# Optimization experiments

Measured on AMD Instinct MI355X. Metric: run time of the kernel, lower is better.

## Reference

```python
import jax, jax.numpy as jnp
import numpy as np

HEADS = 16
DIM_HEAD = 64
SCALE = DIM_HEAD ** -0.5


def setup_inputs() -> dict:
    key = jax.random.key(0)
    ks = jax.random.split(key, 5)
    b, n, dim = 2, 2048, 1024
    inner = HEADS * DIM_HEAD  # 1024
    std = dim ** -0.5
    return {
        "x": jax.random.normal(ks[0], (b, n, dim), jnp.float32),
        "ln_gamma": jnp.ones((dim,), jnp.float32),
        "ln_beta": jnp.zeros((dim,), jnp.float32),
        "W_qk": jax.random.normal(ks[1], (dim, 2 * inner), jnp.float32) * std,
        "W_v": jax.random.normal(ks[2], (dim, inner), jnp.float32) * std,
        "W_out": jax.random.normal(ks[3], (inner, dim), jnp.float32) * std,
        "b_out": jnp.zeros((dim,), jnp.float32),
    }


def _layernorm(x, gamma, beta, eps=1e-5):
    mu = jnp.mean(x, axis=-1, keepdims=True)
    var = jnp.var(x, axis=-1, keepdims=True)
    return (x - mu) * jax.lax.rsqrt(var + eps) * gamma + beta


def reference(x, ln_gamma, ln_beta, W_qk, W_v, W_out, b_out):
    b, n, dim = x.shape
    h, d = HEADS, DIM_HEAD
    xn = _layernorm(x, ln_gamma, ln_beta)
    qk = xn @ W_qk                      # [b, n, 2*h*d]
    q, k = jnp.split(qk, 2, axis=-1)    # each [b, n, h*d]
    v = xn @ W_v                        # [b, n, h*d]
    # b n (h d) -> b h n d
    q = q.reshape(b, n, h, d).transpose(0, 2, 1, 3)
    k = k.reshape(b, n, h, d).transpose(0, 2, 1, 3)
    v = v.reshape(b, n, h, d).transpose(0, 2, 1, 3)
    dots = jnp.einsum('bhid,bhjd->bhij', q, k) * SCALE
    attn = jax.nn.softmax(dots, axis=-1)
    out = jnp.einsum('bhij,bhjd->bhid', attn, v)
    out = out.transpose(0, 2, 1, 3).reshape(b, n, h * d)
    return out @ W_out + b_out
```

## Files before the change

### kernel.cpp

```cpp
#include <hip/hip_runtime.h>

#define HEADS 16
#define DHEAD 64
#define BATCH 2
#define SEQ   2048
#define DIM   1024
#define ROWS  (BATCH*SEQ)
#define SCALE_LOG2E 0.180336880f

typedef short v8s __attribute__((ext_vector_type(8)));
typedef float v4f __attribute__((ext_vector_type(4)));

__device__ __forceinline__ float fast_exp2(float x) {
    return __builtin_amdgcn_exp2f(x);
}

__device__ __forceinline__ unsigned short f2bf(float f) {
    unsigned u = __float_as_uint(f);
    u += 0x7FFFu + ((u >> 16) & 1u);
    return (unsigned short)(u >> 16);
}

__device__ __forceinline__ unsigned pk_bf2(float hi, float lo) {
    return __builtin_amdgcn_perm(__float_as_uint(hi), __float_as_uint(lo), 0x07060302u);
}

#define GLDS16(g, l) __builtin_amdgcn_global_load_lds( \
    (__attribute__((address_space(1))) void*)(g), \
    (__attribute__((address_space(3))) void*)(l), 16, 0, 0)

__global__ __launch_bounds__(256) void ln_kernel(const float* __restrict__ x,
                                                 const float* __restrict__ gamma,
                                                 const float* __restrict__ beta,
                                                 unsigned short* __restrict__ xn) {
    int row = blockIdx.x;
    const float* xr = x + (size_t)row * DIM;
    int t = threadIdx.x;
    float4 v = *(const float4*)(xr + t * 4);
    float s  = v.x + v.y + v.z + v.w;
    float sq = v.x * v.x + v.y * v.y + v.z * v.z + v.w * v.w;
#pragma unroll
    for (int off = 32; off > 0; off >>= 1) {
        s  += __shfl_down(s,  off, 64);
        sq += __shfl_down(sq, off, 64);
    }
    __shared__ float ss[4], ssq[4];
    int wave = t >> 6, lane = t & 63;
    if (lane == 0) { ss[wave] = s; ssq[wave] = sq; }
    __syncthreads();
    float tot  = ss[0] + ss[1] + ss[2] + ss[3];
    float totq = ssq[0] + ssq[1] + ssq[2] + ssq[3];
    float mean = tot * (1.f / DIM);
    float var  = totq * (1.f / DIM) - mean * mean;
    float rstd = rsqrtf(var + 1e-5f);
    float4 g = *(const float4*)(gamma + t * 4);
    float4 bb = *(const float4*)(beta + t * 4);
    ushort4 o;
    o.x = f2bf((v.x - mean) * rstd * g.x + bb.x);
    o.y = f2bf((v.y - mean) * rstd * g.y + bb.y);
    o.z = f2bf((v.z - mean) * rstd * g.z + bb.z);
    o.w = f2bf((v.w - mean) * rstd * g.w + bb.w);
    *(ushort4*)(xn + (size_t)row * DIM + t * 4) = o;
}

__global__ __launch_bounds__(256) void tr_kernel(const float* __restrict__ W,
                                                 unsigned short* __restrict__ Wt,
                                                 int Kw, int Nw) {
    __shared__ float tile[64][65];
    int n0 = blockIdx.x * 64, k0 = blockIdx.y * 64;
    int tid = threadIdx.x;
#pragma unroll
    for (int l = 0; l < 4; ++l) {
        int kk = (tid >> 4) + l * 16;
        int nn = (tid & 15) * 4;
        float4 v = *(const float4*)(W + (size_t)(k0 + kk) * Nw + n0 + nn);
        tile[kk][nn + 0] = v.x; tile[kk][nn + 1] = v.y;
        tile[kk][nn + 2] = v.z; tile[kk][nn + 3] = v.w;
    }
    __syncthreads();
#pragma unroll
    for (int l = 0; l < 4; ++l) {
        int cid = tid + l * 256;
        int nn = cid >> 4, kc = (cid & 15) * 4;
        ushort4 o;
        o.x = f2bf(tile[kc + 0][nn]);
        o.y = f2bf(tile[kc + 1][nn]);
        o.z = f2bf(tile[kc + 2][nn]);
        o.w = f2bf(tile[kc + 3][nn]);
        *(ushort4*)(Wt + (size_t)(n0 + nn) * Kw + k0 + kc) = o;
    }
}

template<int BN>
__device__ __forceinline__ void mm_core2(const unsigned short* __restrict__ A,
                                         const unsigned short* __restrict__ Bt,
                                         int K, int aTile, int bTile,
                                         unsigned short (*As)[32],
                                         unsigned short (*Bs)[32],
                                         v4f (*acc)[4]) {
    constexpr int MI = (BN == 128) ? 4 : 2;
    int t = threadIdx.x;
    int w = t >> 6, L = t & 63, l15 = L & 15, quad = L >> 4;
    int aOff = (BN == 128) ? (w >> 1) * 64 : w * 32;
    int bOff = (BN == 128) ? (w & 1) * 64 : 0;
    int srow = L >> 2, schunk = (L & 3) * 8;
    for (int k0 = 0; k0 < K; k0 += 32) {
        __syncthreads();
#pragma unroll
        for (int j = 0; j < 2; ++j) {
            int g = w * 2 + j;
            GLDS16(A + (size_t)(aTile + g * 16 + srow) * K + k0 + schunk,
                   &As[g * 16][0]);
        }
#pragma unroll
        for (int j = 0; j < BN / 64; ++j) {
            int g = (BN == 128) ? (w * 2 + j) : w;
            GLDS16(Bt + (size_t)(bTile + g * 16 + srow) * K + k0 + schunk,
                   &Bs[g * 16][0]);
        }
        __syncthreads();
        v8s a[MI], b[4];
#pragma unroll
        for (int i = 0; i < MI; ++i) a[i] = *(const v8s*)&As[aOff + i * 16 + l15][quad * 8];
#pragma unroll
        for (int j = 0; j < 4; ++j) b[j] = *(const v8s*)&Bs[bOff + j * 16 + l15][quad * 8];
#pragma unroll
        for (int i = 0; i < MI; ++i)
#pragma unroll
            for (int j = 0; j < 4; ++j)
                acc[i][j] = __builtin_amdgcn_mfma_f32_16x16x32_bf16(a[i], b[j], acc[i][j], 0, 0, 0);
    }
}

__global__ __launch_bounds__(256) void gemm_qk_kernel(const unsigned short* __restrict__ A,
                                                      const unsigned short* __restrict__ Bt,
                                                      unsigned short* __restrict__ q_h,
                                                      unsigned short* __restrict__ k_h) {
    __shared__ __align__(16) unsigned short As[128][32];
    __shared__ __align__(16) unsigned short Bs[128][32];
    int t = threadIdx.x, w = t >> 6, L = t & 63, l15 = L & 15, quad = L >> 4;
    int aTile = blockIdx.y * 128, bTile = blockIdx.x * 128;
    int aOff = (w >> 1) * 64, bOff = (w & 1) * 64;
    v4f acc[4][4] = {};
    mm_core2<128>(A, Bt, DIM, aTile, bTile, As, Bs, acc);
#pragma unroll
    for (int j = 0; j < 4; ++j) {
        int col = bTile + bOff + j * 16 + l15;
        unsigned short* dst = (col < 1024) ? q_h : k_h;
        int c = col & 1023;
        int h = c >> 6, d = c & 63;
#pragma unroll
        for (int i = 0; i < 4; ++i) {
#pragma unroll
            for (int r = 0; r < 4; ++r) {
                int m = aTile + aOff + i * 16 + quad * 4 + r;
                int b = m >> 11, seq = m & 2047;
                dst[(((size_t)(b * 16 + h)) * SEQ + seq) * 64 + d] = f2bf(acc[i][j][r]);
            }
        }
    }
}

__global__ __launch_bounds__(256) void gemm_v_kernel(const unsigned short* __restrict__ A,
                                                     const unsigned short* __restrict__ Bt,
                                                     unsigned short* __restrict__ v_t) {
    __shared__ __align__(16) unsigned short As[128][32];
    __shared__ __align__(16) unsigned short Bs[64][32];
    int t = threadIdx.x, w = t >> 6, L = t & 63, l15 = L & 15, quad = L >> 4;
    int aTile = blockIdx.y * 128, bTile = blockIdx.x * 64;
    v4f acc[2][4] = {};
    mm_core2<64>(A, Bt, DIM, aTile, bTile, As, Bs, acc);
#pragma unroll
    for (int j = 0; j < 4; ++j) {
        int c = bTile + j * 16 + l15;
        int h = c >> 6, d = c & 63;
#pragma unroll
        for (int i = 0; i < 2; ++i) {
            int m0 = aTile + w * 32 + i * 16 + quad * 4;
            int b = m0 >> 11, seq0 = m0 & 2047;
            ushort4 o;
            o.x = f2bf(acc[i][j][0]); o.y = f2bf(acc[i][j][1]);
            o.z = f2bf(acc[i][j][2]); o.w = f2bf(acc[i][j][3]);
            *(ushort4*)(v_t + (((size_t)(b * 16 + h)) * 64 + d) * SEQ + seq0) = o;
        }
    }
}

__global__ __launch_bounds__(256) void gemm_out_kernel(const unsigned short* __restrict__ A,
                                                       const unsigned short* __restrict__ Bt,
                                                       const float* __restrict__ bias,
                                                       float* __restrict__ C) {
    __shared__ __align__(16) unsigned short As[128][32];
    __shared__ __align__(16) unsigned short Bs[64][32];
    int t = threadIdx.x, w = t >> 6, L = t & 63, l15 = L & 15, quad = L >> 4;
    int aTile = blockIdx.y * 128, bTile = blockIdx.x * 64;
    v4f acc[2][4] = {};
    mm_core2<64>(A, Bt, DIM, aTile, bTile, As, Bs, acc);
#pragma unroll
    for (int j = 0; j < 4; ++j) {
        int col = bTile + j * 16 + l15;
        float bv = bias[col];
#pragma unroll
        for (int i = 0; i < 2; ++i)
#pragma unroll
            for (int r = 0; r < 4; ++r) {
                int m = aTile + w * 32 + i * 16 + quad * 4 + r;
                C[(size_t)m * DIM + col] = acc[i][j][r] + bv;
            }
    }
}

__global__ __launch_bounds__(256) void attn_kernel(const unsigned short* __restrict__ q_h,
                                                   const unsigned short* __restrict__ k_h,
                                                   const unsigned short* __restrict__ v_t,
                                                   unsigned short* __restrict__ ao) {
    __shared__ __align__(16) unsigned short KF[8 * 64 * 8];
    __shared__ __align__(16) unsigned short VF[8 * 64 * 8];
    __shared__ __align__(16) unsigned short Pld[4][2][16 * 72];
    int qt = blockIdx.x, h = blockIdx.y, b = blockIdx.z;
    int bh = b * HEADS + h;
    int w = threadIdx.x >> 6;
    int L = threadIdx.x & 63, l15 = L & 15, quad = L >> 4;

    const unsigned short* qp = q_h + ((size_t)bh * SEQ + qt * 128 + w * 32 + l15) * 64 + quad * 8;
    v8s qf[2][2];
    qf[0][0] = *(const v8s*)(qp);
    qf[0][1] = *(const v8s*)(qp + 32);
    qf[1][0] = *(const v8s*)(qp + 16 * 64);
    qf[1][1] = *(const v8s*)(qp + 16 * 64 + 32);

    const unsigned short* kstage = k_h + ((size_t)bh * SEQ + w * 16 + l15) * 64 + quad * 8;
    const unsigned short* vstage = v_t + ((size_t)bh * 64 + w * 16 + l15) * SEQ + quad * 8;

    v4f o[2][4] = {};
    v4f lacc[2] = {};
    const short ob = (short)0x3F80;
    const v8s ones = {ob, ob, ob, ob, ob, ob, ob, ob};

    v8s ks0 = *(const v8s*)(kstage);
    v8s ks1 = *(const v8s*)(kstage + 32);
    v8s vs0 = *(const v8s*)(vstage);
    v8s vs1 = *(const v8s*)(vstage + 32);

    for (int j0 = 0; j0 < SEQ; j0 += 64) {
        __syncthreads();
        *(v8s*)&KF[((w * 2 + 0) * 64 + L) * 8] = ks0;
        *(v8s*)&KF[((w * 2 + 1) * 64 + L) * 8] = ks1;
        *(v8s*)&VF[((w * 2 + 0) * 64 + L) * 8] = vs0;
        *(v8s*)&VF[((w * 2 + 1) * 64 + L) * 8] = vs1;
        __syncthreads();
        if (j0 + 64 < SEQ) {
            ks0 = *(const v8s*)(kstage + (size_t)(j0 + 64) * 64);
            ks1 = *(const v8s*)(kstage + (size_t)(j0 + 64) * 64 + 32);
            vs0 = *(const v8s*)(vstage + j0 + 64);
            vs1 = *(const v8s*)(vstage + j0 + 64 + 32);
        }
        v8s kf[4][2], vf[4][2];
#pragma unroll
        for (int jt = 0; jt < 4; ++jt) {
            kf[jt][0] = *(const v8s*)&KF[((jt * 2 + 0) * 64 + L) * 8];
            kf[jt][1] = *(const v8s*)&KF[((jt * 2 + 1) * 64 + L) * 8];
            vf[jt][0] = *(const v8s*)&VF[((jt * 2 + 0) * 64 + L) * 8];
            vf[jt][1] = *(const v8s*)&VF[((jt * 2 + 1) * 64 + L) * 8];
        }
        v4f s[2][4] = {};
#pragma unroll
        for (int m = 0; m < 2; ++m)
#pragma unroll
            for (int jt = 0; jt < 4; ++jt) {
                s[m][jt] = __builtin_amdgcn_mfma_f32_16x16x32_bf16(kf[jt][0], qf[m][0], s[m][jt], 0, 0, 0);
                s[m][jt] = __builtin_amdgcn_mfma_f32_16x16x32_bf16(kf[jt][1], qf[m][1], s[m][jt], 0, 0, 0);
            }
#pragma unroll
        for (int m = 0; m < 2; ++m)
#pragma unroll
            for (int jt = 0; jt < 4; ++jt) {
                float p0 = fast_exp2(s[m][jt][0] * SCALE_LOG2E);
                float p1 = fast_exp2(s[m][jt][1] * SCALE_LOG2E);
                float p2 = fast_exp2(s[m][jt][2] * SCALE_LOG2E);
                float p3 = fast_exp2(s[m][jt][3] * SCALE_LOG2E);
                uint2 pk;
                pk.x = pk_bf2(p1, p0);
                pk.y = pk_bf2(p3, p2);
                *(uint2*)&Pld[w][m][l15 * 72 + jt * 16 + quad * 4] = pk;
            }
#pragma unroll
        for (int m = 0; m < 2; ++m) {
            v8s pb0 = *(const v8s*)&Pld[w][m][l15 * 72 + quad * 8];
            v8s pb1 = *(const v8s*)&Pld[w][m][l15 * 72 + 32 + quad * 8];
#pragma unroll
            for (int dt = 0; dt < 4; ++dt) {
                o[m][dt] = __builtin_amdgcn_mfma_f32_16x16x32_bf16(vf[dt][0], pb0, o[m][dt], 0, 0, 0);
                o[m][dt] = __builtin_amdgcn_mfma_f32_16x16x32_bf16(vf[dt][1], pb1, o[m][dt], 0, 0, 0);
            }
            lacc[m] = __builtin_amdgcn_mfma_f32_16x16x32_bf16(ones, pb0, lacc[m], 0, 0, 0);
            lacc[m] = __builtin_amdgcn_mfma_f32_16x16x32_bf16(ones, pb1, lacc[m], 0, 0, 0);
        }
    }
#pragma unroll
    for (int m = 0; m < 2; ++m) {
        float inv = 1.f / lacc[m][0];
        int rowg = b * SEQ + qt * 128 + w * 32 + m * 16 + l15;
#pragma unroll
        for (int dt = 0; dt < 4; ++dt) {
            ushort4 ov;
            ov.x = f2bf(o[m][dt][0] * inv);
            ov.y = f2bf(o[m][dt][1] * inv);
            ov.z = f2bf(o[m][dt][2] * inv);
            ov.w = f2bf(o[m][dt][3] * inv);
            *(ushort4*)(ao + (size_t)rowg * DIM + h * 64 + dt * 16 + quad * 4) = ov;
        }
    }
}

extern "C" void kernel_launch(void* const* d_in, const int* in_sizes, int n_in,
                              void* d_out, int out_size, void* d_ws, size_t ws_size,
                              hipStream_t stream) {
    const float* x     = (const float*)d_in[0];
    const float* gamma = (const float*)d_in[1];
    const float* beta  = (const float*)d_in[2];
    const float* Wqk   = (const float*)d_in[3];
    const float* Wv    = (const float*)d_in[4];
    const float* Wout  = (const float*)d_in[5];
    const float* bout  = (const float*)d_in[6];
    float* out = (float*)d_out;

    unsigned short* ws = (unsigned short*)d_ws;
    unsigned short* xn    = ws;
    unsigned short* Wt_qk = xn + (size_t)ROWS * DIM;
    unsigned short* Wt_v  = Wt_qk + (size_t)2048 * DIM;
    unsigned short* Wt_o  = Wt_v + (size_t)DIM * DIM;
    unsigned short* q_h   = Wt_o + (size_t)DIM * DIM;
    unsigned short* k_h   = q_h + (size_t)ROWS * DIM;
    unsigned short* v_t   = k_h + (size_t)ROWS * DIM;
    unsigned short* ao    = v_t + (size_t)ROWS * DIM;

    ln_kernel<<<ROWS, 256, 0, stream>>>(x, gamma, beta, xn);
    tr_kernel<<<dim3(2048 / 64, DIM / 64), 256, 0, stream>>>(Wqk, Wt_qk, DIM, 2048);
    tr_kernel<<<dim3(DIM / 64, DIM / 64), 256, 0, stream>>>(Wv, Wt_v, DIM, DIM);
    tr_kernel<<<dim3(DIM / 64, DIM / 64), 256, 0, stream>>>(Wout, Wt_o, DIM, DIM);
    gemm_qk_kernel<<<dim3(2048 / 128, ROWS / 128), 256, 0, stream>>>(xn, Wt_qk, q_h, k_h);
    gemm_v_kernel<<<dim3(DIM / 64, ROWS / 128), 256, 0, stream>>>(xn, Wt_v, v_t);
    attn_kernel<<<dim3(SEQ / 128, HEADS, BATCH), 256, 0, stream>>>(q_h, k_h, v_t, ao);
    gemm_out_kernel<<<dim3(DIM / 64, ROWS / 128), 256, 0, stream>>>(ao, Wt_o, bout, out);
}
```

Before: 208.5 us.

## Merge weight transposes and QKV GEMMs; swap MFMA operands for vectorized stores

Folds the three weight-transpose launches into one 3D-grid kernel and merges the QK and V projection GEMMs into a single 128x128-tile launch over 3072 columns. This relies on Wt_v sitting directly after Wt_qk in the workspace. For the Q/K and output GEMMs, the MFMA operands are swapped so each lane holds four consecutive columns, which turns scalar bf16/fp32 stores into ushort4/float4 stores. This removes launch overhead and scattered 2-byte and 4-byte writes, at the cost of branchy dispatch and early-exit blocks in the transpose grid.

```diff
diff --git a/kernel.cpp b/kernel.cpp
--- a/kernel.cpp
+++ b/kernel.cpp
@@ -63,11 +63,19 @@
     *(ushort4*)(xn + (size_t)row * DIM + t * 4) = o;
 }
 
-__global__ __launch_bounds__(256) void tr_kernel(const float* __restrict__ W,
-                                                 unsigned short* __restrict__ Wt,
-                                                 int Kw, int Nw) {
+__global__ __launch_bounds__(256) void tr_all_kernel(const float* __restrict__ Wqk,
+                                                     const float* __restrict__ Wv,
+                                                     const float* __restrict__ Wout,
+                                                     unsigned short* __restrict__ Tqk,
+                                                     unsigned short* __restrict__ Tv,
+                                                     unsigned short* __restrict__ To) {
+    int z = blockIdx.z;
+    const float* W = (z == 0) ? Wqk : (z == 1) ? Wv : Wout;
+    unsigned short* Wt = (z == 0) ? Tqk : (z == 1) ? Tv : To;
+    int Nw = (z == 0) ? 2048 : 1024;
+    int n0 = blockIdx.x * 64, k0 = blockIdx.y * 64;
+    if (n0 >= Nw) return;
     __shared__ float tile[64][65];
-    int n0 = blockIdx.x * 64, k0 = blockIdx.y * 64;
     int tid = threadIdx.x;
 #pragma unroll
     for (int l = 0; l < 4; ++l) {
@@ -87,11 +95,11 @@
         o.y = f2bf(tile[kc + 1][nn]);
         o.z = f2bf(tile[kc + 2][nn]);
         o.w = f2bf(tile[kc + 3][nn]);
-        *(ushort4*)(Wt + (size_t)(n0 + nn) * Kw + k0 + kc) = o;
-    }
-}
-
-template<int BN>
+        *(ushort4*)(Wt + (size_t)(n0 + nn) * DIM + k0 + kc) = o;
+    }
+}
+
+template<int BN, bool SWAP>
 __device__ __forceinline__ void mm_core2(const unsigned short* __restrict__ A,
                                          const unsigned short* __restrict__ Bt,
                                          int K, int aTile, int bTile,
@@ -128,60 +136,56 @@
         for (int i = 0; i < MI; ++i)
 #pragma unroll
             for (int j = 0; j < 4; ++j)
-                acc[i][j] = __builtin_amdgcn_mfma_f32_16x16x32_bf16(a[i], b[j], acc[i][j], 0, 0, 0);
-    }
-}
-
-__global__ __launch_bounds__(256) void gemm_qk_kernel(const unsigned short* __restrict__ A,
-                                                      const unsigned short* __restrict__ Bt,
-                                                      unsigned short* __restrict__ q_h,
-                                                      unsigned short* __restrict__ k_h) {
+                acc[i][j] = SWAP
+                    ? __builtin_amdgcn_mfma_f32_16x16x32_bf16(b[j], a[i], acc[i][j], 0, 0, 0)
+                    : __builtin_amdgcn_mfma_f32_16x16x32_bf16(a[i], b[j], acc[i][j], 0, 0, 0);
+    }
+}
+
+__global__ __launch_bounds__(256) void gemm_qkv_kernel(const unsigned short* __restrict__ A,
+                                                       const unsigned short* __restrict__ Bt,
+                                                       unsigned short* __restrict__ q_h,
+                                                       unsigned short* __restrict__ k_h,
+                                                       unsigned short* __restrict__ v_t) {
     __shared__ __align__(16) unsigned short As[128][32];
     __shared__ __align__(16) unsigned short Bs[128][32];
     int t = threadIdx.x, w = t >> 6, L = t & 63, l15 = L & 15, quad = L >> 4;
     int aTile = blockIdx.y * 128, bTile = blockIdx.x * 128;
     int aOff = (w >> 1) * 64, bOff = (w & 1) * 64;
     v4f acc[4][4] = {};
-    mm_core2<128>(A, Bt, DIM, aTile, bTile, As, Bs, acc);
-#pragma unroll
-    for (int j = 0; j < 4; ++j) {
-        int col = bTile + bOff + j * 16 + l15;
-        unsigned short* dst = (col < 1024) ? q_h : k_h;
-        int c = col & 1023;
-        int h = c >> 6, d = c & 63;
-#pragma unroll
-        for (int i = 0; i < 4; ++i) {
-#pragma unroll
-            for (int r = 0; r < 4; ++r) {
-                int m = aTile + aOff + i * 16 + quad * 4 + r;
+    if (bTile < 2048) {
+        mm_core2<128, true>(A, Bt, DIM, aTile, bTile, As, Bs, acc);
+#pragma unroll
+        for (int j = 0; j < 4; ++j) {
+            int col = bTile + bOff + j * 16 + quad * 4;
+            unsigned short* dst = (col < 1024) ? q_h : k_h;
+            int c = col & 1023;
+            int h = c >> 6, d = c & 63;
+#pragma unroll
+            for (int i = 0; i < 4; ++i) {
+                int m = aTile + aOff + i * 16 + l15;
                 int b = m >> 11, seq = m & 2047;
-                dst[(((size_t)(b * 16 + h)) * SEQ + seq) * 64 + d] = f2bf(acc[i][j][r]);
-            }
-        }
-    }
-}
-
-__global__ __launch_bounds__(256) void gemm_v_kernel(const unsigned short* __restrict__ A,
-                                                     const unsigned short* __restrict__ Bt,
-                                                     unsigned short* __restrict__ v_t) {
-    __shared__ __align__(16) unsigned short As[128][32];
-    __shared__ __align__(16) unsigned short Bs[64][32];
-    int t = threadIdx.x, w = t >> 6, L = t & 63, l15 = L & 15, quad = L >> 4;
-    int aTile = blockIdx.y * 128, bTile = blockIdx.x * 64;
-    v4f acc[2][4] = {};
-    mm_core2<64>(A, Bt, DIM, aTile, bTile, As, Bs, acc);
-#pragma unroll
-    for (int j = 0; j < 4; ++j) {
-        int c = bTile + j * 16 + l15;
-        int h = c >> 6, d = c & 63;
-#pragma unroll
-        for (int i = 0; i < 2; ++i) {
-            int m0 = aTile + w * 32 + i * 16 + quad * 4;
-            int b = m0 >> 11, seq0 = m0 & 2047;
-            ushort4 o;
-            o.x = f2bf(acc[i][j][0]); o.y = f2bf(acc[i][j][1]);
-            o.z = f2bf(acc[i][j][2]); o.w = f2bf(acc[i][j][3]);
-            *(ushort4*)(v_t + (((size_t)(b * 16 + h)) * 64 + d) * SEQ + seq0) = o;
+                ushort4 o;
+                o.x = f2bf(acc[i][j][0]); o.y = f2bf(acc[i][j][1]);
+                o.z = f2bf(acc[i][j][2]); o.w = f2bf(acc[i][j][3]);
+                *(ushort4*)(dst + (((size_t)(b * 16 + h)) * SEQ + seq) * 64 + d) = o;
+            }
+        }
+    } else {
+        mm_core2<128, false>(A, Bt, DIM, aTile, bTile, As, Bs, acc);
+#pragma unroll
+        for (int j = 0; j < 4; ++j) {
+            int c = bTile + bOff + j * 16 + l15 - 2048;
+            int h = c >> 6, d = c & 63;
+#pragma unroll
+            for (int i = 0; i < 4; ++i) {
+                int m0 = aTile + aOff + i * 16 + quad * 4;
+                int b = m0 >> 11, seq0 = m0 & 2047;
+                ushort4 o;
+                o.x = f2bf(acc[i][j][0]); o.y = f2bf(acc[i][j][1]);
+                o.z = f2bf(acc[i][j][2]); o.w = f2bf(acc[i][j][3]);
+                *(ushort4*)(v_t + (((size_t)(b * 16 + h)) * 64 + d) * SEQ + seq0) = o;
+            }
         }
     }
 }
@@ -195,18 +199,18 @@
     int t = threadIdx.x, w = t >> 6, L = t & 63, l15 = L & 15, quad = L >> 4;
     int aTile = blockIdx.y * 128, bTile = blockIdx.x * 64;
     v4f acc[2][4] = {};
-    mm_core2<64>(A, Bt, DIM, aTile, bTile, As, Bs, acc);
+    mm_core2<64, true>(A, Bt, DIM, aTile, bTile, As, Bs, acc);
 #pragma unroll
     for (int j = 0; j < 4; ++j) {
-        int col = bTile + j * 16 + l15;
-        float bv = bias[col];
-#pragma unroll
-        for (int i = 0; i < 2; ++i)
-#pragma unroll
-            for (int r = 0; r < 4; ++r) {
-                int m = aTile + w * 32 + i * 16 + quad * 4 + r;
-                C[(size_t)m * DIM + col] = acc[i][j][r] + bv;
-            }
+        int n = bTile + j * 16 + quad * 4;
+        float4 bv = *(const float4*)(bias + n);
+#pragma unroll
+        for (int i = 0; i < 2; ++i) {
+            int m = aTile + w * 32 + i * 16 + l15;
+            float4 o = make_float4(acc[i][j][0] + bv.x, acc[i][j][1] + bv.y,
+                                   acc[i][j][2] + bv.z, acc[i][j][3] + bv.w);
+            *(float4*)(C + (size_t)m * DIM + n) = o;
+        }
     }
 }
 
@@ -336,11 +340,8 @@
     unsigned short* ao    = v_t + (size_t)ROWS * DIM;
 
     ln_kernel<<<ROWS, 256, 0, stream>>>(x, gamma, beta, xn);
-    tr_kernel<<<dim3(2048 / 64, DIM / 64), 256, 0, stream>>>(Wqk, Wt_qk, DIM, 2048);
-    tr_kernel<<<dim3(DIM / 64, DIM / 64), 256, 0, stream>>>(Wv, Wt_v, DIM, DIM);
-    tr_kernel<<<dim3(DIM / 64, DIM / 64), 256, 0, stream>>>(Wout, Wt_o, DIM, DIM);
-    gemm_qk_kernel<<<dim3(2048 / 128, ROWS / 128), 256, 0, stream>>>(xn, Wt_qk, q_h, k_h);
-    gemm_v_kernel<<<dim3(DIM / 64, ROWS / 128), 256, 0, stream>>>(xn, Wt_v, v_t);
+    tr_all_kernel<<<dim3(32, 16, 3), 256, 0, stream>>>(Wqk, Wv, Wout, Wt_qk, Wt_v, Wt_o);
+    gemm_qkv_kernel<<<dim3(3072 / 128, ROWS / 128), 256, 0, stream>>>(xn, Wt_qk, q_h, k_h, v_t);
     attn_kernel<<<dim3(SEQ / 128, HEADS, BATCH), 256, 0, stream>>>(q_h, k_h, v_t, ao);
     gemm_out_kernel<<<dim3(DIM / 64, ROWS / 128), 256, 0, stream>>>(ao, Wt_o, bout, out);
 }
```

After: 194.9 us. -6.5%, faster.
